# Kernel optimization log

Measured on AMD Instinct MI355X. Metric: run time of the kernel, lower is better.

## Reference

```python
import jax, jax.numpy as jnp
import numpy as np

ARCHI = [2048, 2048, 2048, 10]
BATCH = 256
EPS = 0.1          # epsilon step size for OIM dynamics
BETA = 0.5         # nudging factor (forward arg, hardcoded here)
TWO_PI = 6.283185307179586


def setup_inputs() -> dict:
    key = jax.random.key(0)
    ks = jax.random.split(key, 16)

    def lin_w(k, out_d, in_d):
        lim = 1.0 / np.sqrt(in_d)
        return jax.random.uniform(ks[k], (out_d, in_d), jnp.float32, -lim, lim)

    x = jax.random.normal(ks[0], (BATCH, ARCHI[0]), jnp.float32)
    y = jax.random.randint(ks[1], (BATCH,), 0, ARCHI[-1])
    # phases initialised uniformly in [0, 2pi) (random_phase_initialisation=True)
    phi0 = jax.random.uniform(ks[2], (BATCH, ARCHI[1]), jnp.float32) * TWO_PI
    phi1 = jax.random.uniform(ks[3], (BATCH, ARCHI[2]), jnp.float32) * TWO_PI
    phi2 = jax.random.uniform(ks[4], (BATCH, ARCHI[3]), jnp.float32) * TWO_PI
    W0 = lin_w(5, ARCHI[1], ARCHI[0])   # [2048, 2048] (out, in)
    W1 = lin_w(6, ARCHI[2], ARCHI[1])   # [2048, 2048]
    W2 = lin_w(7, ARCHI[3], ARCHI[2])   # [10, 2048]
    # torch inits biases/syncs to zero; use small random values so every
    # energy term contributes non-trivially to the correctness baseline.
    b0 = 0.01 * jax.random.normal(ks[8], (ARCHI[1],), jnp.float32)
    b1 = 0.01 * jax.random.normal(ks[9], (ARCHI[2],), jnp.float32)
    b2 = 0.01 * jax.random.normal(ks[10], (ARCHI[3],), jnp.float32)
    k0 = 0.01 * jax.random.normal(ks[11], (ARCHI[1],), jnp.float32)
    k1 = 0.01 * jax.random.normal(ks[12], (ARCHI[2],), jnp.float32)
    k2 = 0.01 * jax.random.normal(ks[13], (ARCHI[3],), jnp.float32)
    return {"x": x, "W0": W0, "W1": W1, "W2": W2,
            "b0": b0, "b1": b1, "b2": b2,
            "k0": k0, "k1": k1, "k2": k2,
            "phi0": phi0, "phi1": phi1, "phi2": phi2,
            "y": y, "T": 5}


def _energy_sum(x, W0, W1, W2, b0, b1, b2, k0, k1, k2, phases, y1h):
    """Sum over batch of F = E_OIM + beta * L (MSE on cos(phi_out))."""
    phi0, phi1, phi2 = phases
    c0, c1, c2 = jnp.cos(phi0), jnp.cos(phi1), jnp.cos(phi2)
    s0, s1, s2 = jnp.sin(phi0), jnp.sin(phi1), jnp.sin(phi2)
    # input coupling: -sum_j (x W0^T)_j cos(phi0_j)
    e = -jnp.sum((x @ W0.T) * c0, axis=1)
    # hidden coupling: -sum_{i,j} cos(phi_prev_i - phi_next_j) W[j,i]
    # exact decomposition cos(a-b) = cos a cos b + sin a sin b -> fused GEMMs
    e -= jnp.einsum('bi,ji,bj->b', c0, W1, c1) + jnp.einsum('bi,ji,bj->b', s0, W1, s1)
    e -= jnp.einsum('bi,ji,bj->b', c1, W2, c2) + jnp.einsum('bi,ji,bj->b', s1, W2, s2)
    # bias field: -sum_j h_j cos(phi_j)
    e -= c0 @ b0 + c1 @ b1 + c2 @ b2
    # sync (2nd harmonic): -0.5 * sum_j K_j cos(2 phi_j)
    e -= 0.5 * (jnp.cos(2.0 * phi0) @ k0 + jnp.cos(2.0 * phi1) @ k1
                + jnp.cos(2.0 * phi2) @ k2)
    # nudged loss: 0.5 * MSE(cos(phi_out), 2*onehot(y)-1) summed over classes
    loss = 0.5 * jnp.sum((c2 - y1h) ** 2, axis=1)
    return jnp.sum(e + BETA * loss)


def reference(x, W0, W1, W2, b0, b1, b2, k0, k1, k2, phi0, phi1, phi2, y, T):
    y1h = 2.0 * jax.nn.one_hot(y, ARCHI[-1], dtype=jnp.float32) - 1.0
    grad_fn = jax.grad(
        lambda ph: _energy_sum(x, W0, W1, W2, b0, b1, b2, k0, k1, k2, ph, y1h))

    def step(phases, _):
        g = grad_fn(phases)
        return tuple(p - EPS * gi for p, gi in zip(phases, g)), None

    phases, _ = jax.lax.scan(step, (phi0, phi1, phi2), None, length=T)
    # concatenate final phases along feature dim: [B, 2048+2048+10]
    return jnp.concatenate(phases, axis=1)
```

## Files before the change

kernel.cpp:

```cpp
#include <hip/hip_runtime.h>
#include <hip/hip_bf16.h>


#define BATCH 256
#define DIM 2048
#define NCLS 10
#define OUTSTRIDE 4106
#define TSTEPS 5

typedef unsigned short ushort_t;
typedef unsigned int u32;
typedef __attribute__((ext_vector_type(8))) short short8;
typedef __attribute__((ext_vector_type(4))) float f32x4;
typedef __attribute__((ext_vector_type(4))) unsigned short ushort4v;

__device__ __forceinline__ ushort_t f2bf(float f) {
  union { float f; u32 u; } v; v.f = f;
  u32 r = v.u + 0x7FFFu + ((v.u >> 16) & 1u);
  return (ushort_t)(r >> 16);
}

__global__ void setup_all(const float* __restrict__ W0, ushort_t* __restrict__ w0b,
                          const float* __restrict__ x, ushort_t* __restrict__ xb,
                          const float* __restrict__ W2, ushort_t* __restrict__ w2b,
                          const float* __restrict__ W1, ushort_t* __restrict__ w1b,
                          ushort_t* __restrict__ w1tb,
                          const float* __restrict__ phi0, const float* __restrict__ phi1,
                          const float* __restrict__ phi2, float* __restrict__ out,
                          ushort_t* __restrict__ cs0, ushort_t* __restrict__ cs1,
                          float* __restrict__ t2_0) {
  __shared__ float tile[64][65];
  int bid = blockIdx.x;
  int tid = threadIdx.x;
  if (bid < 2048) {
    int i = (bid * 256 + tid) * 8;
#pragma unroll
    for (int h = 0; h < 2; ++h) {
      float4 v = *(const float4*)&W0[i + h * 4];
      ushort4v o;
      o.x = f2bf(v.x); o.y = f2bf(v.y); o.z = f2bf(v.z); o.w = f2bf(v.w);
      *(ushort4v*)&w0b[i + h * 4] = o;
    }
  } else if (bid < 2560) {
    int i = ((bid - 2048) * 256 + tid) * 4;
    float4 v = *(const float4*)&x[i];
    ushort4v o;
    o.x = f2bf(v.x); o.y = f2bf(v.y); o.z = f2bf(v.z); o.w = f2bf(v.w);
    *(ushort4v*)&xb[i] = o;
  } else if (bid < 2688) {
    int i = ((bid - 2560) * 256 + tid) * 4;
    int r = i >> 11;
    ushort4v o;
    if (r < NCLS) {
      float4 v = *(const float4*)&W2[i];
      o.x = f2bf(v.x); o.y = f2bf(v.y); o.z = f2bf(v.z); o.w = f2bf(v.w);
    } else {
      o.x = 0; o.y = 0; o.z = 0; o.w = 0;
    }
    *(ushort4v*)&w2b[i] = o;
  } else if (bid < 3712) {
    int t = bid - 2688;
    int c0 = (t & 31) * 64, r0 = (t >> 5) * 64;
    int tx = tid & 63, ty = tid >> 6;
    for (int r = ty; r < 64; r += 4) {
      float v = W1[(size_t)(r0 + r) * DIM + c0 + tx];
      tile[r][tx] = v;
      w1b[(size_t)(r0 + r) * DIM + c0 + tx] = f2bf(v);
    }
    __syncthreads();
    for (int r = ty; r < 64; r += 4)
      w1tb[(size_t)(c0 + r) * DIM + r0 + tx] = f2bf(tile[tx][r]);
  } else {
    int t = bid - 3712;
    int xx = t % 17, b = t / 17;
    int col = xx * 256 + tid;
    if (col >= OUTSTRIDE) return;
    int rc = (b >> 5) * 64 + (b & 31);
    float phi, s, c;
    if (col < DIM) {
      phi = phi0[(size_t)b * DIM + col];
      __sincosf(phi, &s, &c);
      cs0[(size_t)rc * DIM + col] = f2bf(c);
      cs0[(size_t)(rc + 32) * DIM + col] = f2bf(s);
    } else if (col < 2 * DIM) {
      int j = col - DIM;
      phi = phi1[(size_t)b * DIM + j];
      __sincosf(phi, &s, &c);
      cs1[(size_t)rc * DIM + j] = f2bf(c);
      cs1[(size_t)(rc + 32) * DIM + j] = f2bf(s);
    } else {
      int j = col - 2 * DIM;
      phi = phi2[b * NCLS + j];
      __sincosf(phi, &s, &c);
      t2_0[b * 32 + j] = c;
      t2_0[b * 32 + 16 + j] = s;
    }
    out[(size_t)b * OUTSTRIDE + col] = phi;
  }
}

__device__ __forceinline__ void gload16(const void* g, void* l) {
  __builtin_amdgcn_global_load_lds((const __attribute__((address_space(1))) u32*)g,
                                   (__attribute__((address_space(3))) u32*)l, 16, 0, 0);
}

__global__ __launch_bounds__(256) void gemm_a0(
    const ushort_t* __restrict__ A, const ushort_t* __restrict__ B,
    float* __restrict__ Cp) {
  int ks = blockIdx.z;
  int n0 = blockIdx.x * 64;
  int m0 = blockIdx.y * 64;
  int kbase = ks * 1024;

  __shared__ ushort_t lds[2][2][64 * 64];
  int tid = threadIdx.x, wave = tid >> 6, lane = tid & 63;
  int wr = wave >> 1, wc = wave & 1;

  f32x4 acc[2][2];
#pragma unroll
  for (int m = 0; m < 2; ++m)
#pragma unroll
    for (int n = 0; n < 2; ++n) acc[m][n] = (f32x4)0.f;

  int srow = tid >> 3;
  int sg = tid & 7;

  auto stage = [&](int buf, int k0q) {
#pragma unroll
    for (int rseg = 0; rseg < 2; ++rseg) {
      int row = rseg * 32 + srow;
      int gsrc = (sg ^ (row & 7)) * 8;
      gload16(A + (size_t)(m0 + row) * DIM + k0q + gsrc, &lds[buf][0][row * 64 + sg * 8]);
      gload16(B + (size_t)(n0 + row) * DIM + k0q + gsrc, &lds[buf][1][row * 64 + sg * 8]);
    }
  };

  stage(0, kbase);
  int cur = 0;
  for (int kt = 0; kt < 16; ++kt) {
    if (kt + 1 < 16) {
      stage(cur ^ 1, kbase + (kt + 1) * 64);
      asm volatile("s_waitcnt vmcnt(4)" ::: "memory");
    } else {
      asm volatile("s_waitcnt vmcnt(0)" ::: "memory");
    }
    __builtin_amdgcn_s_barrier();
    const ushort_t* la = lds[cur][0];
    const ushort_t* lb = lds[cur][1];
    int rowa = wr * 32 + (lane & 15);
    int rowb = wc * 32 + (lane & 15);
    int gl = lane >> 4;
#pragma unroll
    for (int kk = 0; kk < 64; kk += 32) {
      int kg = kk >> 3;
      int ga = ((gl + kg) ^ (rowa & 7)) * 8;
      int gb = ((gl + kg) ^ (rowb & 7)) * 8;
      short8 af0 = *(const short8*)&la[rowa * 64 + ga];
      short8 af1 = *(const short8*)&la[(rowa + 16) * 64 + ga];
      short8 bf0 = *(const short8*)&lb[rowb * 64 + gb];
      short8 bf1 = *(const short8*)&lb[(rowb + 16) * 64 + gb];
      acc[0][0] = __builtin_amdgcn_mfma_f32_16x16x32_bf16(af0, bf0, acc[0][0], 0, 0, 0);
      acc[0][1] = __builtin_amdgcn_mfma_f32_16x16x32_bf16(af0, bf1, acc[0][1], 0, 0, 0);
      acc[1][0] = __builtin_amdgcn_mfma_f32_16x16x32_bf16(af1, bf0, acc[1][0], 0, 0, 0);
      acc[1][1] = __builtin_amdgcn_mfma_f32_16x16x32_bf16(af1, bf1, acc[1][1], 0, 0, 0);
    }
    asm volatile("s_waitcnt lgkmcnt(0)" ::: "memory");
    __builtin_amdgcn_s_barrier();
    cur ^= 1;
  }

  float* C = Cp + (size_t)ks * BATCH * DIM;
#pragma unroll
  for (int m = 0; m < 2; ++m)
#pragma unroll
    for (int n = 0; n < 2; ++n)
#pragma unroll
      for (int r = 0; r < 4; ++r) {
        int row = m0 + wr * 32 + m * 16 + (lane >> 4) * 4 + r;
        int col = n0 + wc * 32 + n * 16 + (lane & 15);
        C[(size_t)row * DIM + col] = acc[m][n][r];
      }
}

__global__ __launch_bounds__(256, 3) void fused_iter(
    const ushort_t* __restrict__ cs0_old, const ushort_t* __restrict__ cs1_old,
    ushort_t* __restrict__ cs0_new, ushort_t* __restrict__ cs1_new,
    const ushort_t* __restrict__ w1tb, const ushort_t* __restrict__ w1b,
    const ushort_t* __restrict__ w2b,
    const float* __restrict__ a0p,
    const float* __restrict__ b0, const float* __restrict__ k0,
    const float* __restrict__ b1, const float* __restrict__ k1,
    const float* __restrict__ b2, const float* __restrict__ k2,
    const float* __restrict__ W2, const int* __restrict__ y,
    const float* __restrict__ t2_old, float* __restrict__ t2_new,
    float* __restrict__ out) {
  int z = blockIdx.z;
  if (z == 0 && blockIdx.x != 0) return;
  const ushort_t* A = (z == 2) ? cs0_old : cs1_old;
  const ushort_t* B = (z == 0) ? w2b : (z == 1 ? w1tb : w1b);
  int n0 = blockIdx.x * 64;
  int g = blockIdx.y;
  int m0 = g * 64;

  __shared__ ushort_t lds[2][2][64 * 64];
  int tid = threadIdx.x, wave = tid >> 6, lane = tid & 63;
  int wr = wave >> 1, wc = wave & 1;

  f32x4 acc[2][2];
#pragma unroll
  for (int m = 0; m < 2; ++m)
#pragma unroll
    for (int n = 0; n < 2; ++n) acc[m][n] = (f32x4)0.f;

  int srow = tid >> 3;
  int sg = tid & 7;

  auto stage = [&](int buf, int k0q) {
#pragma unroll
    for (int rseg = 0; rseg < 2; ++rseg) {
      int row = rseg * 32 + srow;
      int gsrc = (sg ^ (row & 7)) * 8;
      gload16(A + (size_t)(m0 + row) * DIM + k0q + gsrc, &lds[buf][0][row * 64 + sg * 8]);
      gload16(B + (size_t)(n0 + row) * DIM + k0q + gsrc, &lds[buf][1][row * 64 + sg * 8]);
    }
  };

  stage(0, 0);
  int cur = 0;
  for (int kt = 0; kt < 32; ++kt) {
    if (kt + 1 < 32) {
      stage(cur ^ 1, (kt + 1) * 64);
      asm volatile("s_waitcnt vmcnt(4)" ::: "memory");
    } else {
      asm volatile("s_waitcnt vmcnt(0)" ::: "memory");
    }
    __builtin_amdgcn_s_barrier();
    const ushort_t* la = lds[cur][0];
    const ushort_t* lb = lds[cur][1];
    int rowa = wr * 32 + (lane & 15);
    int rowb = wc * 32 + (lane & 15);
    int gl = lane >> 4;
#pragma unroll
    for (int kk = 0; kk < 64; kk += 32) {
      int kg = kk >> 3;
      int ga = ((gl + kg) ^ (rowa & 7)) * 8;
      int gb = ((gl + kg) ^ (rowb & 7)) * 8;
      short8 af0 = *(const short8*)&la[rowa * 64 + ga];
      short8 af1 = *(const short8*)&la[(rowa + 16) * 64 + ga];
      short8 bf0 = *(const short8*)&lb[rowb * 64 + gb];
      short8 bf1 = *(const short8*)&lb[(rowb + 16) * 64 + gb];
      acc[0][0] = __builtin_amdgcn_mfma_f32_16x16x32_bf16(af0, bf0, acc[0][0], 0, 0, 0);
      acc[0][1] = __builtin_amdgcn_mfma_f32_16x16x32_bf16(af0, bf1, acc[0][1], 0, 0, 0);
      acc[1][0] = __builtin_amdgcn_mfma_f32_16x16x32_bf16(af1, bf0, acc[1][0], 0, 0, 0);
      acc[1][1] = __builtin_amdgcn_mfma_f32_16x16x32_bf16(af1, bf1, acc[1][1], 0, 0, 0);
    }
    asm volatile("s_waitcnt lgkmcnt(0)" ::: "memory");
    __builtin_amdgcn_s_barrier();
    cur ^= 1;
  }

  float* ldsF = (float*)lds;
#pragma unroll
  for (int m = 0; m < 2; ++m)
#pragma unroll
    for (int n = 0; n < 2; ++n)
#pragma unroll
      for (int r = 0; r < 4; ++r)
        ldsF[(wr * 32 + m * 16 + (lane >> 4) * 4 + r) * 65 +
             wc * 32 + n * 16 + (lane & 15)] = acc[m][n][r];
  __syncthreads();

  int c4 = (tid & 15) * 4;
  int jg = n0 + c4;

  if (z == 0) {
    if (c4 < 12) {
#pragma unroll
      for (int bb = 0; bb < 2; ++bb) {
        int bl = (tid >> 4) * 2 + bb;
        int b = g * 32 + bl;
        int yb = y[b];
#pragma unroll
        for (int i = 0; i < 4; ++i) {
          int j = c4 + i;
          if (j < NCLS) {
            float u2c = ldsF[bl * 65 + j];
            float u2s = ldsF[(bl + 32) * 65 + j];
            size_t oi = (size_t)b * OUTSTRIDE + 2 * DIM + j;
            float phi = out[oi];
            float s, c;
            __sincosf(phi, &s, &c);
            float y1h = (yb == j) ? 1.f : -1.f;
            float gr = (u2c + b2[j]) * s - u2s * c + k2[j] * 2.f * s * c
                       - 0.5f * (c - y1h) * s;
            float pn = phi - 0.1f * gr;
            out[oi] = pn;
            __sincosf(pn, &s, &c);
            t2_new[b * 32 + j] = c;
            t2_new[b * 32 + 16 + j] = s;
          }
        }
      }
    }
    return;
  }

  ushort_t* csn = (z == 1) ? cs0_new : cs1_new;
  const float* bb_ = (z == 1) ? b0 : b1;
  const float* kk_ = (z == 1) ? k0 : k1;
  f32x4 bv = *(const f32x4*)&bb_[jg];
  f32x4 kv = *(const f32x4*)&kk_[jg];
  size_t oofs = (z == 1) ? 0 : (size_t)DIM;

#pragma unroll
  for (int bb = 0; bb < 2; ++bb) {
    int bl = (tid >> 4) * 2 + bb;
    int b = g * 32 + bl;
    f32x4 P, Q;
#pragma unroll
    for (int i = 0; i < 4; ++i) {
      P[i] = ldsF[bl * 65 + c4 + i];
      Q[i] = ldsF[(bl + 32) * 65 + c4 + i];
    }
    f32x4 uc, us;
    if (z == 1) {
      f32x4 av = *(const f32x4*)&a0p[(size_t)b * DIM + jg];
      f32x4 av1 = *(const f32x4*)&a0p[(size_t)BATCH * DIM + (size_t)b * DIM + jg];
      av += av1;
      uc = P + av + bv;
      us = Q;
    } else {
      f32x4 tc = (f32x4)0.f, ts = (f32x4)0.f;
#pragma unroll
      for (int q = 0; q < NCLS; ++q) {
        f32x4 wv = *(const f32x4*)&W2[q * DIM + jg];
        tc += t2_old[b * 32 + q] * wv;
        ts += t2_old[b * 32 + 16 + q] * wv;
      }
      uc = P + tc + bv;
      us = Q + ts;
    }
    float* po = &out[(size_t)b * OUTSTRIDE + oofs + jg];
    f32x4 ph = *(const f32x4*)po;
    ushort4v cv, sv;
#pragma unroll
    for (int i = 0; i < 4; ++i) {
      float s, c;
      __sincosf(ph[i], &s, &c);
      float gr = uc[i] * s - us[i] * c + kv[i] * 2.f * s * c;
      float pn = ph[i] - 0.1f * gr;
      ph[i] = pn;
      __sincosf(pn, &s, &c);
      cv[i] = f2bf(c);
      sv[i] = f2bf(s);
    }
    *(f32x4*)po = ph;
    int rc = g * 64 + bl;
    *(ushort4v*)&csn[(size_t)rc * DIM + jg] = cv;
    *(ushort4v*)&csn[(size_t)(rc + 32) * DIM + jg] = sv;
  }
}

extern "C" void kernel_launch(void* const* d_in, const int* in_sizes, int n_in,
                              void* d_out, int out_size, void* d_ws, size_t ws_size,
                              hipStream_t stream) {
  const float* x    = (const float*)d_in[0];
  const float* W0   = (const float*)d_in[1];
  const float* W1   = (const float*)d_in[2];
  const float* W2   = (const float*)d_in[3];
  const float* b0   = (const float*)d_in[4];
  const float* b1   = (const float*)d_in[5];
  const float* b2   = (const float*)d_in[6];
  const float* k0   = (const float*)d_in[7];
  const float* k1   = (const float*)d_in[8];
  const float* k2   = (const float*)d_in[9];
  const float* phi0 = (const float*)d_in[10];
  const float* phi1 = (const float*)d_in[11];
  const float* phi2 = (const float*)d_in[12];
  const int*   y    = (const int*)d_in[13];
  float* out = (float*)d_out;

  const size_t CS = (size_t)2 * BATCH * DIM;

  char* w = (char*)d_ws;
  ushort_t* w0b  = (ushort_t*)w; w += (size_t)DIM * DIM * 2;
  ushort_t* w1b  = (ushort_t*)w; w += (size_t)DIM * DIM * 2;
  ushort_t* w1tb = (ushort_t*)w; w += (size_t)DIM * DIM * 2;
  ushort_t* w2b  = (ushort_t*)w; w += (size_t)64 * DIM * 2;
  ushort_t* xb   = (ushort_t*)w; w += (size_t)BATCH * DIM * 2;
  ushort_t* csi0 = (ushort_t*)w; w += 2 * CS * 2;
  ushort_t* csi1 = (ushort_t*)w; w += 2 * CS * 2;
  float* a0p = (float*)w; w += (size_t)2 * BATCH * DIM * 4;
  float* t2  = (float*)w; w += (size_t)2 * BATCH * 32 * 4;

  setup_all<<<8064, 256, 0, stream>>>(W0, w0b, x, xb, W2, w2b, W1, w1b, w1tb,
                                      phi0, phi1, phi2, out, csi0, csi1, t2);

  gemm_a0<<<dim3(32, 4, 2), 256, 0, stream>>>(xb, w0b, a0p);

  for (int t = 0; t < TSTEPS; ++t) {
    int r = t & 1, wv = r ^ 1;
    fused_iter<<<dim3(32, 8, 3), 256, 0, stream>>>(
        csi0 + r * CS, csi1 + r * CS, csi0 + wv * CS, csi1 + wv * CS,
        w1tb, w1b, w2b, a0p, b0, k0, b1, k1, b2, k2, W2, y,
        t2 + r * BATCH * 32, t2 + wv * BATCH * 32, out);
  }
}
```

Baseline: 133.9 us.

## Split-K across waves in fused_iter and fold the output-layer GEMM into it

The fused iteration kernel now uses 128-wide K tiles, with each wave covering a 32-element K slice of a full 64x64 output tile (4x4 MFMA fragments per wave). Partial sums are then reduced across waves through LDS. The separate z=0 output-layer grid slice is removed: the 10-class u2 product is computed by the blocks with blockIdx.z==0, x==0, reusing their A fragments with a padded 16-row W2 buffer. This cuts the wasted blocks and halves the K-loop iterations, in exchange for more registers (occupancy hint lowered from 3 to 2), larger LDS use, and an extra reduction and serial tail in the u2 blocks.

After: 140.5 us. 5.0% more time.

```diff
diff --git a/kernel.cpp b/kernel.cpp
--- a/kernel.cpp
+++ b/kernel.cpp
@@ -47,7 +47,7 @@
     ushort4v o;
     o.x = f2bf(v.x); o.y = f2bf(v.y); o.z = f2bf(v.z); o.w = f2bf(v.w);
     *(ushort4v*)&xb[i] = o;
-  } else if (bid < 2688) {
+  } else if (bid < 2592) {
     int i = ((bid - 2560) * 256 + tid) * 4;
     int r = i >> 11;
     ushort4v o;
@@ -58,8 +58,8 @@
       o.x = 0; o.y = 0; o.z = 0; o.w = 0;
     }
     *(ushort4v*)&w2b[i] = o;
-  } else if (bid < 3712) {
-    int t = bid - 2688;
+  } else if (bid < 3616) {
+    int t = bid - 2592;
     int c0 = (t & 31) * 64, r0 = (t >> 5) * 64;
     int tx = tid & 63, ty = tid >> 6;
     for (int r = ty; r < 64; r += 4) {
@@ -71,7 +71,7 @@
     for (int r = ty; r < 64; r += 4)
       w1tb[(size_t)(c0 + r) * DIM + r0 + tx] = f2bf(tile[tx][r]);
   } else {
-    int t = bid - 3712;
+    int t = bid - 3616;
     int xx = t % 17, b = t / 17;
     int col = xx * 256 + tid;
     if (col >= OUTSTRIDE) return;
@@ -104,6 +104,11 @@
                                    (__attribute__((address_space(3))) u32*)l, 16, 0, 0);
 }
 
+__device__ __forceinline__ float rd(const float* S, int row, int col) {
+  return S[((row >> 4) * 4 + (col >> 4)) * 256 +
+           ((((row >> 2) & 3) * 16 + (col & 15)) << 2) + (row & 3)];
+}
+
 __global__ __launch_bounds__(256) void gemm_a0(
     const ushort_t* __restrict__ A, const ushort_t* __restrict__ B,
     float* __restrict__ Cp) {
@@ -182,7 +187,7 @@
       }
 }
 
-__global__ __launch_bounds__(256, 3) void fused_iter(
+__global__ __launch_bounds__(256, 2) void fused_iter(
     const ushort_t* __restrict__ cs0_old, const ushort_t* __restrict__ cs1_old,
     ushort_t* __restrict__ cs0_new, ushort_t* __restrict__ cs1_new,
     const ushort_t* __restrict__ w1tb, const ushort_t* __restrict__ w1b,
@@ -194,136 +199,133 @@
     const float* __restrict__ W2, const int* __restrict__ y,
     const float* __restrict__ t2_old, float* __restrict__ t2_new,
     float* __restrict__ out) {
-  int z = blockIdx.z;
-  if (z == 0 && blockIdx.x != 0) return;
-  const ushort_t* A = (z == 2) ? cs0_old : cs1_old;
-  const ushort_t* B = (z == 0) ? w2b : (z == 1 ? w1tb : w1b);
-  int n0 = blockIdx.x * 64;
-  int g = blockIdx.y;
-  int m0 = g * 64;
-
-  __shared__ ushort_t lds[2][2][64 * 64];
+  const int zz = blockIdx.z;
+  const ushort_t* A = zz ? cs0_old : cs1_old;
+  const ushort_t* B = zz ? w1b : w1tb;
+  const int n0 = blockIdx.x * 64;
+  const int g = blockIdx.y;
+  const int m0 = g * 64;
+  const bool dou2 = (zz == 0) && (blockIdx.x == 0);
+
+  __shared__ ushort_t lds[2][2][64 * 128];
   int tid = threadIdx.x, wave = tid >> 6, lane = tid & 63;
-  int wr = wave >> 1, wc = wave & 1;
-
-  f32x4 acc[2][2];
-#pragma unroll
-  for (int m = 0; m < 2; ++m)
-#pragma unroll
-    for (int n = 0; n < 2; ++n) acc[m][n] = (f32x4)0.f;
-
-  int srow = tid >> 3;
-  int sg = tid & 7;
-
+  int fr = lane & 15, fq = lane >> 4;
+  int kofs = wave * 32;
+
+  f32x4 acc[4][4];
+#pragma unroll
+  for (int m = 0; m < 4; ++m)
+#pragma unroll
+    for (int n = 0; n < 4; ++n) acc[m][n] = (f32x4)0.f;
+  f32x4 u2acc[4];
+#pragma unroll
+  for (int m = 0; m < 4; ++m) u2acc[m] = (f32x4)0.f;
+  short8 u2b_cur = {}, u2b_nxt = {};
+
+  int srow16 = tid >> 4;
+  int sgran = tid & 15;
   auto stage = [&](int buf, int k0q) {
 #pragma unroll
-    for (int rseg = 0; rseg < 2; ++rseg) {
-      int row = rseg * 32 + srow;
-      int gsrc = (sg ^ (row & 7)) * 8;
-      gload16(A + (size_t)(m0 + row) * DIM + k0q + gsrc, &lds[buf][0][row * 64 + sg * 8]);
-      gload16(B + (size_t)(n0 + row) * DIM + k0q + gsrc, &lds[buf][1][row * 64 + sg * 8]);
+    for (int i = 0; i < 4; ++i) {
+      int row = srow16 + i * 16;
+      int gsrc = (sgran ^ (row & 15)) * 8;
+      gload16(A + (size_t)(m0 + row) * DIM + k0q + gsrc,
+              &lds[buf][0][row * 128 + sgran * 8]);
+      gload16(B + (size_t)(n0 + row) * DIM + k0q + gsrc,
+              &lds[buf][1][row * 128 + sgran * 8]);
     }
   };
 
   stage(0, 0);
+  if (dou2) u2b_cur = *(const short8*)&w2b[fr * 2048 + kofs + fq * 8];
+
   int cur = 0;
-  for (int kt = 0; kt < 32; ++kt) {
-    if (kt + 1 < 32) {
-      stage(cur ^ 1, (kt + 1) * 64);
-      asm volatile("s_waitcnt vmcnt(4)" ::: "memory");
+  for (int kt = 0; kt < 16; ++kt) {
+    if (kt + 1 < 16) {
+      stage(cur ^ 1, (kt + 1) * 128);
+      if (dou2) {
+        u2b_nxt = *(const short8*)&w2b[fr * 2048 + (kt + 1) * 128 + kofs + fq * 8];
+        __builtin_amdgcn_sched_barrier(0);
+        asm volatile("s_waitcnt vmcnt(9)" ::: "memory");
+      } else {
+        asm volatile("s_waitcnt vmcnt(8)" ::: "memory");
+      }
     } else {
       asm volatile("s_waitcnt vmcnt(0)" ::: "memory");
     }
     __builtin_amdgcn_s_barrier();
     const ushort_t* la = lds[cur][0];
     const ushort_t* lb = lds[cur][1];
-    int rowa = wr * 32 + (lane & 15);
-    int rowb = wc * 32 + (lane & 15);
-    int gl = lane >> 4;
-#pragma unroll
-    for (int kk = 0; kk < 64; kk += 32) {
-      int kg = kk >> 3;
-      int ga = ((gl + kg) ^ (rowa & 7)) * 8;
-      int gb = ((gl + kg) ^ (rowb & 7)) * 8;
-      short8 af0 = *(const short8*)&la[rowa * 64 + ga];
-      short8 af1 = *(const short8*)&la[(rowa + 16) * 64 + ga];
-      short8 bf0 = *(const short8*)&lb[rowb * 64 + gb];
-      short8 bf1 = *(const short8*)&lb[(rowb + 16) * 64 + gb];
-      acc[0][0] = __builtin_amdgcn_mfma_f32_16x16x32_bf16(af0, bf0, acc[0][0], 0, 0, 0);
-      acc[0][1] = __builtin_amdgcn_mfma_f32_16x16x32_bf16(af0, bf1, acc[0][1], 0, 0, 0);
-      acc[1][0] = __builtin_amdgcn_mfma_f32_16x16x32_bf16(af1, bf0, acc[1][0], 0, 0, 0);
-      acc[1][1] = __builtin_amdgcn_mfma_f32_16x16x32_bf16(af1, bf1, acc[1][1], 0, 0, 0);
+    short8 af[4], bf[4];
+#pragma unroll
+    for (int m = 0; m < 4; ++m) {
+      int row = m * 16 + fr;
+      int gk = (kofs >> 3) + fq;
+      int o = row * 128 + ((gk ^ (row & 15)) << 3);
+      af[m] = *(const short8*)&la[o];
+      bf[m] = *(const short8*)&lb[o];
+    }
+#pragma unroll
+    for (int m = 0; m < 4; ++m)
+#pragma unroll
+      for (int n = 0; n < 4; ++n)
+        acc[m][n] = __builtin_amdgcn_mfma_f32_16x16x32_bf16(af[m], bf[n], acc[m][n], 0, 0, 0);
+    if (dou2) {
+#pragma unroll
+      for (int m = 0; m < 4; ++m)
+        u2acc[m] = __builtin_amdgcn_mfma_f32_16x16x32_bf16(af[m], u2b_cur, u2acc[m], 0, 0, 0);
+      u2b_cur = u2b_nxt;
     }
     asm volatile("s_waitcnt lgkmcnt(0)" ::: "memory");
     __builtin_amdgcn_s_barrier();
     cur ^= 1;
   }
 
-  float* ldsF = (float*)lds;
-#pragma unroll
-  for (int m = 0; m < 2; ++m)
-#pragma unroll
-    for (int n = 0; n < 2; ++n)
-#pragma unroll
-      for (int r = 0; r < 4; ++r)
-        ldsF[(wr * 32 + m * 16 + (lane >> 4) * 4 + r) * 65 +
-             wc * 32 + n * 16 + (lane & 15)] = acc[m][n][r];
+  float* S = (float*)lds;
+#pragma unroll
+  for (int m = 0; m < 4; ++m)
+#pragma unroll
+    for (int n = 0; n < 4; ++n)
+      *(f32x4*)&S[wave * 4096 + (m * 4 + n) * 256 + lane * 4] = acc[m][n];
   __syncthreads();
+#pragma unroll
+  for (int j = 0; j < 4; ++j) {
+    int o = j * 1024 + tid * 4;
+    f32x4 v = *(f32x4*)&S[o];
+    v += *(f32x4*)&S[4096 + o];
+    v += *(f32x4*)&S[8192 + o];
+    v += *(f32x4*)&S[12288 + o];
+    *(f32x4*)&S[o] = v;
+  }
+  __syncthreads();
+
+  if (dou2) {
+#pragma unroll
+    for (int m = 0; m < 4; ++m)
+      *(f32x4*)&S[4096 + wave * 1024 + m * 256 + lane * 4] = u2acc[m];
+  }
 
   int c4 = (tid & 15) * 4;
   int jg = n0 + c4;
-
-  if (z == 0) {
-    if (c4 < 12) {
-#pragma unroll
-      for (int bb = 0; bb < 2; ++bb) {
-        int bl = (tid >> 4) * 2 + bb;
-        int b = g * 32 + bl;
-        int yb = y[b];
-#pragma unroll
-        for (int i = 0; i < 4; ++i) {
-          int j = c4 + i;
-          if (j < NCLS) {
-            float u2c = ldsF[bl * 65 + j];
-            float u2s = ldsF[(bl + 32) * 65 + j];
-            size_t oi = (size_t)b * OUTSTRIDE + 2 * DIM + j;
-            float phi = out[oi];
-            float s, c;
-            __sincosf(phi, &s, &c);
-            float y1h = (yb == j) ? 1.f : -1.f;
-            float gr = (u2c + b2[j]) * s - u2s * c + k2[j] * 2.f * s * c
-                       - 0.5f * (c - y1h) * s;
-            float pn = phi - 0.1f * gr;
-            out[oi] = pn;
-            __sincosf(pn, &s, &c);
-            t2_new[b * 32 + j] = c;
-            t2_new[b * 32 + 16 + j] = s;
-          }
-        }
-      }
-    }
-    return;
-  }
-
-  ushort_t* csn = (z == 1) ? cs0_new : cs1_new;
-  const float* bb_ = (z == 1) ? b0 : b1;
-  const float* kk_ = (z == 1) ? k0 : k1;
+  const float* bb_ = zz ? b1 : b0;
+  const float* kk_ = zz ? k1 : k0;
   f32x4 bv = *(const f32x4*)&bb_[jg];
   f32x4 kv = *(const f32x4*)&kk_[jg];
-  size_t oofs = (z == 1) ? 0 : (size_t)DIM;
-
-#pragma unroll
-  for (int bb = 0; bb < 2; ++bb) {
-    int bl = (tid >> 4) * 2 + bb;
+  size_t oofs = zz ? (size_t)DIM : 0;
+  ushort_t* csn = zz ? cs1_new : cs0_new;
+
+#pragma unroll
+  for (int bb2 = 0; bb2 < 2; ++bb2) {
+    int bl = (tid >> 4) * 2 + bb2;
     int b = g * 32 + bl;
     f32x4 P, Q;
 #pragma unroll
     for (int i = 0; i < 4; ++i) {
-      P[i] = ldsF[bl * 65 + c4 + i];
-      Q[i] = ldsF[(bl + 32) * 65 + c4 + i];
+      P[i] = rd(S, bl, c4 + i);
+      Q[i] = rd(S, bl + 32, c4 + i);
     }
     f32x4 uc, us;
-    if (z == 1) {
+    if (zz == 0) {
       f32x4 av = *(const f32x4*)&a0p[(size_t)b * DIM + jg];
       f32x4 av1 = *(const f32x4*)&a0p[(size_t)BATCH * DIM + (size_t)b * DIM + jg];
       av += av1;
@@ -358,6 +360,38 @@
     int rc = g * 64 + bl;
     *(ushort4v*)&csn[(size_t)rc * DIM + jg] = cv;
     *(ushort4v*)&csn[(size_t)(rc + 32) * DIM + jg] = sv;
+  }
+
+  if (dou2) {
+    __syncthreads();
+    {
+      int o = 4096 + tid * 4;
+      f32x4 v = *(f32x4*)&S[o];
+      v += *(f32x4*)&S[o + 1024];
+      v += *(f32x4*)&S[o + 2048];
+      v += *(f32x4*)&S[o + 3072];
+      *(f32x4*)&S[o] = v;
+    }
+    __syncthreads();
+    for (int it = tid; it < 32 * NCLS; it += 256) {
+      int bl = it / NCLS, j = it % NCLS;
+      int b = g * 32 + bl;
+      float u2c = S[4096 + ((bl >> 4) * 256) + ((((bl >> 2) & 3) * 16 + j) << 2) + (bl & 3)];
+      int bl2 = bl + 32;
+      float u2s = S[4096 + ((bl2 >> 4) * 256) + ((((bl2 >> 2) & 3) * 16 + j) << 2) + (bl2 & 3)];
+      size_t oi = (size_t)b * OUTSTRIDE + 2 * DIM + j;
+      float phi = out[oi];
+      float s, c;
+      __sincosf(phi, &s, &c);
+      float y1h = (y[b] == j) ? 1.f : -1.f;
+      float gr = (u2c + b2[j]) * s - u2s * c + k2[j] * 2.f * s * c
+                 - 0.5f * (c - y1h) * s;
+      float pn = phi - 0.1f * gr;
+      out[oi] = pn;
+      __sincosf(pn, &s, &c);
+      t2_new[b * 32 + j] = c;
+      t2_new[b * 32 + 16 + j] = s;
+    }
   }
 }
 
@@ -386,21 +420,21 @@
   ushort_t* w0b  = (ushort_t*)w; w += (size_t)DIM * DIM * 2;
   ushort_t* w1b  = (ushort_t*)w; w += (size_t)DIM * DIM * 2;
   ushort_t* w1tb = (ushort_t*)w; w += (size_t)DIM * DIM * 2;
-  ushort_t* w2b  = (ushort_t*)w; w += (size_t)64 * DIM * 2;
+  ushort_t* w2b  = (ushort_t*)w; w += (size_t)16 * DIM * 2;
   ushort_t* xb   = (ushort_t*)w; w += (size_t)BATCH * DIM * 2;
   ushort_t* csi0 = (ushort_t*)w; w += 2 * CS * 2;
   ushort_t* csi1 = (ushort_t*)w; w += 2 * CS * 2;
   float* a0p = (float*)w; w += (size_t)2 * BATCH * DIM * 4;
   float* t2  = (float*)w; w += (size_t)2 * BATCH * 32 * 4;
 
-  setup_all<<<8064, 256, 0, stream>>>(W0, w0b, x, xb, W2, w2b, W1, w1b, w1tb,
+  setup_all<<<7968, 256, 0, stream>>>(W0, w0b, x, xb, W2, w2b, W1, w1b, w1tb,
                                       phi0, phi1, phi2, out, csi0, csi1, t2);
 
   gemm_a0<<<dim3(32, 4, 2), 256, 0, stream>>>(xb, w0b, a0p);
 
   for (int t = 0; t < TSTEPS; ++t) {
     int r = t & 1, wv = r ^ 1;
-    fused_iter<<<dim3(32, 8, 3), 256, 0, stream>>>(
+    fused_iter<<<dim3(32, 8, 2), 256, 0, stream>>>(
         csi0 + r * CS, csi1 + r * CS, csi0 + wv * CS, csi1 + wv * CS,
         w1tb, w1b, w2b, a0p, b0, k0, b1, k1, b2, k2, W2, y,
         t2 + r * BATCH * 32, t2 + wv * BATCH * 32, out);
```

## Fold output-layer u2 GEMM into hidden-layer blocks and remap grid to 1D

Applied to the files above, without the earlier changes.

Drops the separate z==0 slice of blocks that computed the 10-class output GEMM on a padded 64-row W2 tile. The output coupling is now computed inside selected hidden-layer blocks by extra MFMAs, using W2 fragments streamed from global memory into registers, and the phase update for the output layer runs in their epilogue. The grid becomes a 1D launch of 512 blocks with a swizzled index mapping, W2's bf16 copy shrinks to 16 rows, and launch bounds drop to 2 waves per SIMD. The goal is to remove the launch-slot and tail cost of the output slice, at the price of extra load and MFMA work on a few blocks and lower occupancy.

Measured after the change: 162.8 us. 21.6% more time.

```diff
diff --git a/kernel.cpp b/kernel.cpp
--- a/kernel.cpp
+++ b/kernel.cpp
@@ -47,7 +47,7 @@
     ushort4v o;
     o.x = f2bf(v.x); o.y = f2bf(v.y); o.z = f2bf(v.z); o.w = f2bf(v.w);
     *(ushort4v*)&xb[i] = o;
-  } else if (bid < 2688) {
+  } else if (bid < 2592) {
     int i = ((bid - 2560) * 256 + tid) * 4;
     int r = i >> 11;
     ushort4v o;
@@ -58,8 +58,8 @@
       o.x = 0; o.y = 0; o.z = 0; o.w = 0;
     }
     *(ushort4v*)&w2b[i] = o;
-  } else if (bid < 3712) {
-    int t = bid - 2688;
+  } else if (bid < 3616) {
+    int t = bid - 2592;
     int c0 = (t & 31) * 64, r0 = (t >> 5) * 64;
     int tx = tid & 63, ty = tid >> 6;
     for (int r = ty; r < 64; r += 4) {
@@ -71,7 +71,7 @@
     for (int r = ty; r < 64; r += 4)
       w1tb[(size_t)(c0 + r) * DIM + r0 + tx] = f2bf(tile[tx][r]);
   } else {
-    int t = bid - 3712;
+    int t = bid - 3616;
     int xx = t % 17, b = t / 17;
     int col = xx * 256 + tid;
     if (col >= OUTSTRIDE) return;
@@ -182,7 +182,7 @@
       }
 }
 
-__global__ __launch_bounds__(256, 3) void fused_iter(
+__global__ __launch_bounds__(256, 2) void fused_iter(
     const ushort_t* __restrict__ cs0_old, const ushort_t* __restrict__ cs1_old,
     ushort_t* __restrict__ cs0_new, ushort_t* __restrict__ cs1_new,
     const ushort_t* __restrict__ w1tb, const ushort_t* __restrict__ w1b,
@@ -194,23 +194,31 @@
     const float* __restrict__ W2, const int* __restrict__ y,
     const float* __restrict__ t2_old, float* __restrict__ t2_new,
     float* __restrict__ out) {
-  int z = blockIdx.z;
-  if (z == 0 && blockIdx.x != 0) return;
-  const ushort_t* A = (z == 2) ? cs0_old : cs1_old;
-  const ushort_t* B = (z == 0) ? w2b : (z == 1 ? w1tb : w1b);
-  int n0 = blockIdx.x * 64;
-  int g = blockIdx.y;
-  int m0 = g * 64;
-
-  __shared__ ushort_t lds[2][2][64 * 64];
+  const int bid = blockIdx.x;
+  const int x8 = bid & 7, s = bid >> 3;
+  const int zz = x8 >> 2, r = x8 & 3;
+  const int xx = r * 8 + (s & 7);
+  const int g = s >> 3;
+  const int n0 = xx * 64, m0 = g * 64;
+  const bool dou2 = (zz == 0) && (xx == 8 * (g & 3));
+
+  const ushort_t* A = zz ? cs0_old : cs1_old;
+  const ushort_t* B = zz ? w1b : w1tb;
+
+  __shared__ ushort_t lds[2][2][4096];
   int tid = threadIdx.x, wave = tid >> 6, lane = tid & 63;
   int wr = wave >> 1, wc = wave & 1;
+  int fr = lane & 15, fq = lane >> 4;
+  const bool u2w = dou2 && (wc == 0);
 
   f32x4 acc[2][2];
 #pragma unroll
   for (int m = 0; m < 2; ++m)
 #pragma unroll
     for (int n = 0; n < 2; ++n) acc[m][n] = (f32x4)0.f;
+  f32x4 u2acc[2];
+  u2acc[0] = (f32x4)0.f; u2acc[1] = (f32x4)0.f;
+  short8 u2c0 = {}, u2c1 = {}, u2n0 = {}, u2n1 = {};
 
   int srow = tid >> 3;
   int sg = tid & 7;
@@ -226,25 +234,35 @@
   };
 
   stage(0, 0);
+  if (u2w) {
+    u2c0 = *(const short8*)&w2b[fr * 2048 + fq * 8];
+    u2c1 = *(const short8*)&w2b[fr * 2048 + 32 + fq * 8];
+  }
   int cur = 0;
   for (int kt = 0; kt < 32; ++kt) {
     if (kt + 1 < 32) {
       stage(cur ^ 1, (kt + 1) * 64);
-      asm volatile("s_waitcnt vmcnt(4)" ::: "memory");
+      if (u2w) {
+        u2n0 = *(const short8*)&w2b[fr * 2048 + (kt + 1) * 64 + fq * 8];
+        u2n1 = *(const short8*)&w2b[fr * 2048 + (kt + 1) * 64 + 32 + fq * 8];
+        __builtin_amdgcn_sched_barrier(0);
+        asm volatile("s_waitcnt vmcnt(6)" ::: "memory");
+      } else {
+        asm volatile("s_waitcnt vmcnt(4)" ::: "memory");
+      }
     } else {
       asm volatile("s_waitcnt vmcnt(0)" ::: "memory");
     }
     __builtin_amdgcn_s_barrier();
     const ushort_t* la = lds[cur][0];
     const ushort_t* lb = lds[cur][1];
-    int rowa = wr * 32 + (lane & 15);
-    int rowb = wc * 32 + (lane & 15);
-    int gl = lane >> 4;
+    int rowa = wr * 32 + fr;
+    int rowb = wc * 32 + fr;
 #pragma unroll
     for (int kk = 0; kk < 64; kk += 32) {
       int kg = kk >> 3;
-      int ga = ((gl + kg) ^ (rowa & 7)) * 8;
-      int gb = ((gl + kg) ^ (rowb & 7)) * 8;
+      int ga = ((fq + kg) ^ (rowa & 7)) * 8;
+      int gb = ((fq + kg) ^ (rowb & 7)) * 8;
       short8 af0 = *(const short8*)&la[rowa * 64 + ga];
       short8 af1 = *(const short8*)&la[(rowa + 16) * 64 + ga];
       short8 bf0 = *(const short8*)&lb[rowb * 64 + gb];
@@ -253,7 +271,13 @@
       acc[0][1] = __builtin_amdgcn_mfma_f32_16x16x32_bf16(af0, bf1, acc[0][1], 0, 0, 0);
       acc[1][0] = __builtin_amdgcn_mfma_f32_16x16x32_bf16(af1, bf0, acc[1][0], 0, 0, 0);
       acc[1][1] = __builtin_amdgcn_mfma_f32_16x16x32_bf16(af1, bf1, acc[1][1], 0, 0, 0);
-    }
+      if (u2w) {
+        short8 ub = kk ? u2c1 : u2c0;
+        u2acc[0] = __builtin_amdgcn_mfma_f32_16x16x32_bf16(af0, ub, u2acc[0], 0, 0, 0);
+        u2acc[1] = __builtin_amdgcn_mfma_f32_16x16x32_bf16(af1, ub, u2acc[1], 0, 0, 0);
+      }
+    }
+    if (u2w) { u2c0 = u2n0; u2c1 = u2n1; }
     asm volatile("s_waitcnt lgkmcnt(0)" ::: "memory");
     __builtin_amdgcn_s_barrier();
     cur ^= 1;
@@ -265,56 +289,27 @@
 #pragma unroll
     for (int n = 0; n < 2; ++n)
 #pragma unroll
-      for (int r = 0; r < 4; ++r)
-        ldsF[(wr * 32 + m * 16 + (lane >> 4) * 4 + r) * 65 +
-             wc * 32 + n * 16 + (lane & 15)] = acc[m][n][r];
+      for (int rr = 0; rr < 4; ++rr)
+        ldsF[(wr * 32 + m * 16 + fq * 4 + rr) * 65 + wc * 32 + n * 16 + fr] = acc[m][n][rr];
+  if (u2w) {
+#pragma unroll
+    for (int m = 0; m < 2; ++m)
+      *(f32x4*)&ldsF[4352 + ((wr * 2 + m) * 64 + lane) * 4] = u2acc[m];
+  }
   __syncthreads();
 
-  int c4 = (tid & 15) * 4;
+  int c4 = fr * 4;
   int jg = n0 + c4;
-
-  if (z == 0) {
-    if (c4 < 12) {
-#pragma unroll
-      for (int bb = 0; bb < 2; ++bb) {
-        int bl = (tid >> 4) * 2 + bb;
-        int b = g * 32 + bl;
-        int yb = y[b];
-#pragma unroll
-        for (int i = 0; i < 4; ++i) {
-          int j = c4 + i;
-          if (j < NCLS) {
-            float u2c = ldsF[bl * 65 + j];
-            float u2s = ldsF[(bl + 32) * 65 + j];
-            size_t oi = (size_t)b * OUTSTRIDE + 2 * DIM + j;
-            float phi = out[oi];
-            float s, c;
-            __sincosf(phi, &s, &c);
-            float y1h = (yb == j) ? 1.f : -1.f;
-            float gr = (u2c + b2[j]) * s - u2s * c + k2[j] * 2.f * s * c
-                       - 0.5f * (c - y1h) * s;
-            float pn = phi - 0.1f * gr;
-            out[oi] = pn;
-            __sincosf(pn, &s, &c);
-            t2_new[b * 32 + j] = c;
-            t2_new[b * 32 + 16 + j] = s;
-          }
-        }
-      }
-    }
-    return;
-  }
-
-  ushort_t* csn = (z == 1) ? cs0_new : cs1_new;
-  const float* bb_ = (z == 1) ? b0 : b1;
-  const float* kk_ = (z == 1) ? k0 : k1;
+  const float* bb_ = zz ? b1 : b0;
+  const float* kk_ = zz ? k1 : k0;
   f32x4 bv = *(const f32x4*)&bb_[jg];
   f32x4 kv = *(const f32x4*)&kk_[jg];
-  size_t oofs = (z == 1) ? 0 : (size_t)DIM;
-
-#pragma unroll
-  for (int bb = 0; bb < 2; ++bb) {
-    int bl = (tid >> 4) * 2 + bb;
+  size_t oofs = zz ? (size_t)DIM : 0;
+  ushort_t* csn = zz ? cs1_new : cs0_new;
+
+#pragma unroll
+  for (int bb2 = 0; bb2 < 2; ++bb2) {
+    int bl = (tid >> 4) * 2 + bb2;
     int b = g * 32 + bl;
     f32x4 P, Q;
 #pragma unroll
@@ -323,7 +318,7 @@
       Q[i] = ldsF[(bl + 32) * 65 + c4 + i];
     }
     f32x4 uc, us;
-    if (z == 1) {
+    if (zz == 0) {
       f32x4 av = *(const f32x4*)&a0p[(size_t)b * DIM + jg];
       f32x4 av1 = *(const f32x4*)&a0p[(size_t)BATCH * DIM + (size_t)b * DIM + jg];
       av += av1;
@@ -345,19 +340,43 @@
     ushort4v cv, sv;
 #pragma unroll
     for (int i = 0; i < 4; ++i) {
-      float s, c;
-      __sincosf(ph[i], &s, &c);
-      float gr = uc[i] * s - us[i] * c + kv[i] * 2.f * s * c;
+      float sn, cn;
+      __sincosf(ph[i], &sn, &cn);
+      float gr = uc[i] * sn - us[i] * cn + kv[i] * 2.f * sn * cn;
       float pn = ph[i] - 0.1f * gr;
       ph[i] = pn;
-      __sincosf(pn, &s, &c);
-      cv[i] = f2bf(c);
-      sv[i] = f2bf(s);
+      __sincosf(pn, &sn, &cn);
+      cv[i] = f2bf(cn);
+      sv[i] = f2bf(sn);
     }
     *(f32x4*)po = ph;
     int rc = g * 64 + bl;
     *(ushort4v*)&csn[(size_t)rc * DIM + jg] = cv;
     *(ushort4v*)&csn[(size_t)(rc + 32) * DIM + jg] = sv;
+  }
+
+  if (dou2) {
+    for (int it = tid; it < 32 * NCLS; it += 256) {
+      int bl = it / NCLS, j = it % NCLS;
+      int b = g * 32 + bl;
+      int r1 = bl, r2 = bl + 32;
+      float u2c = ldsF[4352 + (((r1 >> 5) * 2 + ((r1 >> 4) & 1)) * 64 +
+                               ((r1 >> 2) & 3) * 16 + j) * 4 + (r1 & 3)];
+      float u2s = ldsF[4352 + (((r2 >> 5) * 2 + ((r2 >> 4) & 1)) * 64 +
+                               ((r2 >> 2) & 3) * 16 + j) * 4 + (r2 & 3)];
+      size_t oi = (size_t)b * OUTSTRIDE + 2 * DIM + j;
+      float phi = out[oi];
+      float sn, cn;
+      __sincosf(phi, &sn, &cn);
+      float y1h = (y[b] == j) ? 1.f : -1.f;
+      float gr = (u2c + b2[j]) * sn - u2s * cn + k2[j] * 2.f * sn * cn
+                 - 0.5f * (cn - y1h) * sn;
+      float pn = phi - 0.1f * gr;
+      out[oi] = pn;
+      __sincosf(pn, &sn, &cn);
+      t2_new[b * 32 + j] = cn;
+      t2_new[b * 32 + 16 + j] = sn;
+    }
   }
 }
 
@@ -386,21 +405,21 @@
   ushort_t* w0b  = (ushort_t*)w; w += (size_t)DIM * DIM * 2;
   ushort_t* w1b  = (ushort_t*)w; w += (size_t)DIM * DIM * 2;
   ushort_t* w1tb = (ushort_t*)w; w += (size_t)DIM * DIM * 2;
-  ushort_t* w2b  = (ushort_t*)w; w += (size_t)64 * DIM * 2;
+  ushort_t* w2b  = (ushort_t*)w; w += (size_t)16 * DIM * 2;
   ushort_t* xb   = (ushort_t*)w; w += (size_t)BATCH * DIM * 2;
   ushort_t* csi0 = (ushort_t*)w; w += 2 * CS * 2;
   ushort_t* csi1 = (ushort_t*)w; w += 2 * CS * 2;
   float* a0p = (float*)w; w += (size_t)2 * BATCH * DIM * 4;
   float* t2  = (float*)w; w += (size_t)2 * BATCH * 32 * 4;
 
-  setup_all<<<8064, 256, 0, stream>>>(W0, w0b, x, xb, W2, w2b, W1, w1b, w1tb,
+  setup_all<<<7968, 256, 0, stream>>>(W0, w0b, x, xb, W2, w2b, W1, w1b, w1tb,
                                       phi0, phi1, phi2, out, csi0, csi1, t2);
 
   gemm_a0<<<dim3(32, 4, 2), 256, 0, stream>>>(xb, w0b, a0p);
 
   for (int t = 0; t < TSTEPS; ++t) {
     int r = t & 1, wv = r ^ 1;
-    fused_iter<<<dim3(32, 8, 3), 256, 0, stream>>>(
+    fused_iter<<<512, 256, 0, stream>>>(
         csi0 + r * CS, csi1 + r * CS, csi0 + wv * CS, csi1 + wv * CS,
         w1tb, w1b, w2b, a0p, b0, k0, b1, k1, b2, k2, W2, y,
         t2 + r * BATCH * 32, t2 + wv * BATCH * 32, out);
```
